# Kernel optimization log

Hardware: AMD Instinct MI355X
Metric: run time of the kernel (lower is better)

## Reference

```python
import jax, jax.numpy as jnp
import numpy as np
import math

B, S, H = 8, 1024, 1024
LN_EPS = 1e-5  # assumed epsilon of create_normalization_layer('layer_norm')


def setup_inputs() -> dict:
    key = jax.random.key(0)
    ks = jax.random.split(key, 6)
    context = jax.random.normal(ks[0], (B, S, H), dtype=jnp.float32)
    mask = jnp.ones((B, 1, S), dtype=jnp.int32)
    prior = jax.random.uniform(ks[1], (B, S, S), dtype=jnp.float32)
    # LayerNorm params
    gamma = jnp.ones((H,), dtype=jnp.float32)
    beta = jnp.zeros((H,), dtype=jnp.float32)
    # Dense projections (Glorot-like init)
    scale = 1.0 / np.sqrt(H)
    Wk = jax.random.normal(ks[2], (H, H), dtype=jnp.float32) * scale
    bk = jnp.zeros((H,), dtype=jnp.float32)
    Wq = jax.random.normal(ks[3], (H, H), dtype=jnp.float32) * scale
    bq = jnp.zeros((H,), dtype=jnp.float32)
    return {"context": context, "mask": mask, "prior": prior,
            "gamma": gamma, "beta": beta, "Wk": Wk, "bk": bk, "Wq": Wq, "bq": bq}


def reference(context, mask, prior, gamma, beta, Wk, bk, Wq, bq):
    dtype = context.dtype
    s = context.shape[1]
    hs = context.shape[2]
    i = jnp.arange(s)
    adj_upper = i[:, None] == (i[None, :] - 1)          # [S,S] superdiagonal
    adj_lower = i[:, None] == (i[None, :] + 1)          # subdiagonal
    adj_mask = adj_upper | adj_lower
    pad = mask[:, 0, :].astype(bool)                    # [B,S]
    pad2d = pad[:, :, None] & pad[:, None, :]           # [B,S,S]
    final_adj = adj_mask[None, :, :] & pad2d

    # LayerNorm over last axis
    mu = jnp.mean(context, axis=-1, keepdims=True)
    var = jnp.mean(jnp.square(context - mu), axis=-1, keepdims=True)
    cn = (context - mu) * jax.lax.rsqrt(var + LN_EPS) * gamma + beta

    k = cn @ Wk + bk                                    # [B,S,H]
    q = cn @ Wq + bq
    scores = jnp.einsum('bsh,bth->bst', q, k) / math.sqrt(hs)
    scores = jnp.where(final_adj, scores, jnp.asarray(-1e9, dtype))
    neibor = jax.nn.softmax(scores, axis=-1)
    neibor = jnp.sqrt(neibor * jnp.swapaxes(neibor, 1, 2) + 1e-9)
    neibor = prior + (1.0 - prior) * neibor

    triu = i[None, :] >= i[:, None]                     # [S,S] upper incl diag
    tri = triu.astype(dtype)
    b_eye = jnp.eye(s, dtype=bool)

    t = jnp.log(neibor + 1e-9)
    t = jnp.where(adj_upper[None, :, :], t, jnp.asarray(0.0, dtype))
    t = jnp.einsum('bij,jk->bik', t, tri)               # cumulative over cols
    g = jnp.exp(jnp.einsum('ij,bjk->bik', tri, t))      # hierarchical prefix product
    keep = jnp.logical_not(jnp.logical_xor(triu, b_eye))
    g = jnp.where(keep[None, :, :], g, jnp.asarray(0.0, dtype))
    neibor_diag = jnp.where(b_eye[None, :, :], jnp.asarray(1e-9, dtype), neibor)
    g = g + jnp.swapaxes(g, 1, 2) + neibor_diag
    g = g / (jnp.sum(g, axis=-1, keepdims=True) + 1e-9)

    f2d = pad2d.astype(dtype)
    g = g * f2d
    neibor = neibor * f2d
    return g, neibor
```

## Files before the change

### kernel.cpp

```cpp
#include <hip/hip_runtime.h>
#include <hip/hip_bf16.h>

#define SB 8
#define SS 1024
#define SH 1024
#define LN_EPS 1e-5f

typedef unsigned short u16;
typedef __attribute__((ext_vector_type(8))) short bf16x8;
typedef __attribute__((ext_vector_type(4))) float f32x4;

__device__ __forceinline__ u16 f2bf(float f) {
  __hip_bfloat16 h = __float2bfloat16(f);
  return *reinterpret_cast<u16*>(&h);
}
__device__ __forceinline__ float bf2f(u16 x) {
  unsigned v = ((unsigned)x) << 16;
  return __builtin_bit_cast(float, v);
}

__device__ __forceinline__ void gld16(const void* g, void* l) {
  __builtin_amdgcn_global_load_lds(
      (const __attribute__((address_space(1))) void*)g,
      (__attribute__((address_space(3))) void*)l, 16, 0, 0);
}

__global__ __launch_bounds__(256) void ln_cast(const float* __restrict__ x,
                                               const float* __restrict__ gamma,
                                               const float* __restrict__ beta,
                                               u16* __restrict__ cnb) {
  const int r = blockIdx.x;
  const int t = threadIdx.x;
  const int wave = t >> 6, lane = t & 63;
  const float* xr = x + (size_t)r * SH;
  float4 v = *(const float4*)(xr + 4 * t);

  __shared__ float p1[4], p2[4];
  float s = v.x + v.y + v.z + v.w;
#pragma unroll
  for (int off = 32; off > 0; off >>= 1) s += __shfl_down(s, off, 64);
  if (lane == 0) p1[wave] = s;
  __syncthreads();
  const float mu = (p1[0] + p1[1] + p1[2] + p1[3]) * (1.0f / SH);

  float d0 = v.x - mu, d1 = v.y - mu, d2 = v.z - mu, d3 = v.w - mu;
  float ss = d0 * d0 + d1 * d1 + d2 * d2 + d3 * d3;
#pragma unroll
  for (int off = 32; off > 0; off >>= 1) ss += __shfl_down(ss, off, 64);
  if (lane == 0) p2[wave] = ss;
  __syncthreads();
  const float rstd = rsqrtf((p2[0] + p2[1] + p2[2] + p2[3]) * (1.0f / SH) + LN_EPS);

  float4 gm = *(const float4*)(gamma + 4 * t);
  float4 bt = *(const float4*)(beta + 4 * t);
  ushort4 o;
  o.x = f2bf(d0 * rstd * gm.x + bt.x);
  o.y = f2bf(d1 * rstd * gm.y + bt.y);
  o.z = f2bf(d2 * rstd * gm.z + bt.z);
  o.w = f2bf(d3 * rstd * gm.w + bt.w);
  *(ushort4*)(cnb + (size_t)r * SH + 4 * t) = o;
}

__global__ __launch_bounds__(256) void wcast(const float* __restrict__ Wq,
                                             const float* __restrict__ Wk,
                                             u16* __restrict__ Wq_bf,
                                             u16* __restrict__ Wk_bf) {
  const size_t e = ((size_t)blockIdx.x * 256 + threadIdx.x) * 4;
  const size_t M = (size_t)SH * SH;
  const float* src;
  u16* dst;
  if (e < M) { src = Wq + e; dst = Wq_bf + e; }
  else       { src = Wk + (e - M); dst = Wk_bf + (e - M); }
  float4 v = *(const float4*)src;
  ushort4 o;
  o.x = f2bf(v.x); o.y = f2bf(v.y); o.z = f2bf(v.z); o.w = f2bf(v.w);
  *(ushort4*)dst = o;
}

__global__ __launch_bounds__(256) void wkbq_kernel(const float* __restrict__ Wk,
                                                   const float* __restrict__ bq,
                                                   float* __restrict__ wkbq) {
  const int wave = threadIdx.x >> 6, lane = threadIdx.x & 63;
  const int h = blockIdx.x * 4 + wave;
  const float* row = Wk + (size_t)h * SH;
  float s = 0.f;
#pragma unroll
  for (int v = 0; v < 4; ++v) {
    const int j = v * 256 + lane * 4;
    float4 w = *(const float4*)(row + j);
    float4 b = *(const float4*)(bq + j);
    s += w.x * b.x + w.y * b.y + w.z * b.z + w.w * b.w;
  }
#pragma unroll
  for (int off = 32; off > 0; off >>= 1) s += __shfl_down(s, off, 64);
  if (lane == 0) wkbq[h] = s;
}

__global__ __launch_bounds__(256) void zero_f32(float* __restrict__ p) {
  *(float4*)(p + ((size_t)blockIdx.x * 256 + threadIdx.x) * 4) =
      make_float4(0.f, 0.f, 0.f, 0.f);
}

#define BM 128
#define BN 128
#define BK 32
#define GK 1024
#define GN 1024

__global__ __launch_bounds__(256) void gemm_pt(const u16* __restrict__ A,
                                               const u16* __restrict__ Bt,
                                               u16* __restrict__ C) {
  __shared__ u16 As[BM * BK];
  __shared__ u16 Bs[BN * BK];
  const int tid = threadIdx.x;
  const int m0 = blockIdx.y * BM;
  const int n0 = blockIdx.x * BN;
  const int wave = tid >> 6, lane = tid & 63;
  const int wm = (wave & 1) * 64, wn = (wave >> 1) * 64;
  const int l15 = lane & 15, q = lane >> 4;

  f32x4 acc[4][4] = {};

  const int srow = tid >> 2;
  const int scol = 8 * (tid & 3);
  const u16* gA = A + (size_t)(m0 + srow) * GK + scol;
  const u16* gB = Bt + (size_t)(n0 + srow) * GK + scol;
  u16* lA = &As[srow * BK + scol];
  u16* lB = &Bs[srow * BK + scol];

  for (int k0 = 0; k0 < GK; k0 += BK) {
    __syncthreads();
    gld16(gA + k0, lA);
    gld16(gA + (size_t)64 * GK + k0, lA + 64 * BK);
    gld16(gB + k0, lB);
    gld16(gB + (size_t)64 * GK + k0, lB + 64 * BK);
    __syncthreads();

    bf16x8 af[4], bfr[4];
#pragma unroll
    for (int fm = 0; fm < 4; ++fm)
      af[fm] = *(const bf16x8*)&As[(wm + fm * 16 + l15) * BK + q * 8];
#pragma unroll
    for (int fn = 0; fn < 4; ++fn)
      bfr[fn] = *(const bf16x8*)&Bs[(wn + fn * 16 + l15) * BK + q * 8];
#pragma unroll
    for (int fm = 0; fm < 4; ++fm)
#pragma unroll
      for (int fn = 0; fn < 4; ++fn)
        acc[fm][fn] = __builtin_amdgcn_mfma_f32_16x16x32_bf16(
            af[fm], bfr[fn], acc[fm][fn], 0, 0, 0);
  }

#pragma unroll
  for (int fm = 0; fm < 4; ++fm)
#pragma unroll
    for (int fn = 0; fn < 4; ++fn) {
      const int row0 = m0 + wm + fm * 16 + q * 4;
      const int col = n0 + wn + fn * 16 + l15;
#pragma unroll
      for (int r = 0; r < 4; ++r)
        C[(size_t)(row0 + r) * GN + col] = f2bf(acc[fm][fn][r]);
    }
}

__global__ __launch_bounds__(256) void ugemm_fused(const u16* __restrict__ A,
                                                   const u16* __restrict__ Bt,
                                                   const u16* __restrict__ cnb,
                                                   float* __restrict__ du,
                                                   float* __restrict__ dd) {
  __shared__ u16 As[BM * BK];
  __shared__ u16 Bs[BN * BK];
  const int tid = threadIdx.x;
  const int m0 = blockIdx.y * BM;
  const int n0 = blockIdx.x * BN;
  const int wave = tid >> 6, lane = tid & 63;
  const int wm = (wave & 1) * 64, wn = (wave >> 1) * 64;
  const int l15 = lane & 15, q = lane >> 4;

  f32x4 acc[4][4] = {};

  const int srow = tid >> 2;
  const int scol = 8 * (tid & 3);
  const u16* gA = A + (size_t)(m0 + srow) * GK + scol;
  const u16* gB = Bt + (size_t)(n0 + srow) * GK + scol;
  u16* lA = &As[srow * BK + scol];
  u16* lB = &Bs[srow * BK + scol];

  for (int k0 = 0; k0 < GK; k0 += BK) {
    __syncthreads();
    gld16(gA + k0, lA);
    gld16(gA + (size_t)64 * GK + k0, lA + 64 * BK);
    gld16(gB + k0, lB);
    gld16(gB + (size_t)64 * GK + k0, lB + 64 * BK);
    __syncthreads();

    bf16x8 af[4], bfr[4];
#pragma unroll
    for (int fm = 0; fm < 4; ++fm)
      af[fm] = *(const bf16x8*)&As[(wm + fm * 16 + l15) * BK + q * 8];
#pragma unroll
    for (int fn = 0; fn < 4; ++fn)
      bfr[fn] = *(const bf16x8*)&Bs[(wn + fn * 16 + l15) * BK + q * 8];
#pragma unroll
    for (int fm = 0; fm < 4; ++fm)
#pragma unroll
      for (int fn = 0; fn < 4; ++fn)
        acc[fm][fn] = __builtin_amdgcn_mfma_f32_16x16x32_bf16(
            af[fm], bfr[fn], acc[fm][fn], 0, 0, 0);
  }

#pragma unroll
  for (int fm = 0; fm < 4; ++fm) {
#pragma unroll
    for (int rr = 0; rr < 4; ++rr) {
      const int r = m0 + wm + fm * 16 + q * 4 + rr;
      const int sl = r & (SS - 1);
      float sdu = 0.f, sdd = 0.f;
#pragma unroll
      for (int fn = 0; fn < 4; ++fn) {
        const int col = n0 + wn + fn * 16 + l15;
        const float a = acc[fm][fn][rr];
        if (sl < SS - 1) sdu += a * bf2f(cnb[(size_t)(r + 1) * SH + col]);
        if (sl > 0)      sdd += a * bf2f(cnb[(size_t)(r - 1) * SH + col]);
      }
#pragma unroll
      for (int m = 1; m < 16; m <<= 1) {
        sdu += __shfl_xor(sdu, m, 64);
        sdd += __shfl_xor(sdd, m, 64);
      }
      if (l15 == 0) {
        atomicAdd(&du[r], sdu);
        atomicAdd(&dd[r], sdd);
      }
    }
  }
}

__global__ __launch_bounds__(256) void wdot(const u16* __restrict__ cnb,
                                            const float* __restrict__ wkbq,
                                            float* __restrict__ wvec) {
  const int wave = threadIdx.x >> 6, lane = threadIdx.x & 63;
  const int r = blockIdx.x * 4 + wave;
  const u16* row = cnb + (size_t)r * SH;
  float s = 0.f;
#pragma unroll
  for (int v = 0; v < 4; ++v) {
    const int j = v * 256 + lane * 4;
    ushort4 c = *(const ushort4*)(row + j);
    float4 w = *(const float4*)(wkbq + j);
    s += bf2f(c.x) * w.x + bf2f(c.y) * w.y + bf2f(c.z) * w.z + bf2f(c.w) * w.w;
  }
#pragma unroll
  for (int off = 32; off > 0; off >>= 1) s += __shfl_down(s, off, 64);
  if (lane == 0) wvec[r] = s;
}

__global__ __launch_bounds__(256) void softmax2(const float* __restrict__ du,
                                                const float* __restrict__ dd,
                                                const float* __restrict__ wvec,
                                                float* __restrict__ pup,
                                                float* __restrict__ pdn) {
  const int r = blockIdx.x * 256 + threadIdx.x;
  const int s = r & (SS - 1);
  const bool has_up = (s < SS - 1), has_dn = (s > 0);
  const float scale = 0.03125f;
  float pu, pd;
  if (!has_dn) { pu = 1.f; pd = 0.f; }
  else if (!has_up) { pu = 0.f; pd = 1.f; }
  else {
    const float a = (du[r] + wvec[r + 1]) * scale;
    const float b = (dd[r] + wvec[r - 1]) * scale;
    const float m = fmaxf(a, b);
    const float eu = __expf(a - m), ed = __expf(b - m);
    const float inv = 1.f / (eu + ed);
    pu = eu * inv;
    pd = ed * inv;
  }
  pup[r] = pu;
  pdn[r] = pd;
}

__global__ __launch_bounds__(256) void rows_kernel(const float* __restrict__ prior,
                                                   const int* __restrict__ mask,
                                                   const float* __restrict__ pup,
                                                   const float* __restrict__ pdn,
                                                   float* __restrict__ g_out,
                                                   float* __restrict__ ne_out) {
  const int r = blockIdx.x;
  const int b = r >> 10, i = r & (SS - 1);
  const int t = threadIdx.x;
  const int wave = t >> 6, lane = t & 63;
  const float nbz = 3.1622776601683795e-5f;
  const float nb_im1 = (i >= 1) ? sqrtf(pup[r - 1] * pdn[r] + 1e-9f) : nbz;
  const float nb_ip1 = (i <= SS - 2) ? sqrtf(pup[r] * pdn[r + 1] + 1e-9f) : nbz;

  const float* prow = prior + (size_t)r * SS;
  float4 pr = *(const float4*)(prow + 4 * t);
  const int* mrow = mask + b * SS;
  const float padi = (mrow[i] != 0) ? 1.f : 0.f;
  int4 mk = *(const int4*)(mrow + 4 * t);

  float ne[4], gsum = 0.f;
#pragma unroll
  for (int v = 0; v < 4; ++v) {
    const int k = 4 * t + v;
    const float p = (&pr.x)[v];
    const float nb = (k == i - 1) ? nb_im1 : (k == i + 1) ? nb_ip1 : nbz;
    const float n = p + (1.f - p) * nb;
    ne[v] = n;
    gsum += (k == i) ? (2.f + 1e-9f) : (1.f + n);
  }

  __shared__ float part[4];
#pragma unroll
  for (int off = 32; off > 0; off >>= 1) gsum += __shfl_down(gsum, off, 64);
  if (lane == 0) part[wave] = gsum;
  __syncthreads();
  const float inv = 1.f / (part[0] + part[1] + part[2] + part[3] + 1e-9f);

  float4 go, no;
#pragma unroll
  for (int v = 0; v < 4; ++v) {
    const int k = 4 * t + v;
    const float padk = ((&mk.x)[v] != 0) ? 1.f : 0.f;
    const float f2 = padi * padk;
    const float gt = (k == i) ? (2.f + 1e-9f) : (1.f + ne[v]);
    (&go.x)[v] = gt * inv * f2;
    (&no.x)[v] = ne[v] * f2;
  }
  *(float4*)(g_out + (size_t)r * SS + 4 * t) = go;
  *(float4*)(ne_out + (size_t)r * SS + 4 * t) = no;
}

extern "C" void kernel_launch(void* const* d_in, const int* in_sizes, int n_in,
                              void* d_out, int out_size, void* d_ws, size_t ws_size,
                              hipStream_t stream) {
  const float* context = (const float*)d_in[0];
  const int* mask = (const int*)d_in[1];
  const float* prior = (const float*)d_in[2];
  const float* gamma = (const float*)d_in[3];
  const float* beta = (const float*)d_in[4];
  const float* Wk = (const float*)d_in[5];
  const float* bk = (const float*)d_in[6];
  const float* Wq = (const float*)d_in[7];
  const float* bq = (const float*)d_in[8];
  (void)bk;

  float* out_g = (float*)d_out;
  float* out_n = out_g + (size_t)SB * SS * SS;

  char* ws = (char*)d_ws;
  u16* cnb = (u16*)ws;
  u16* Wq_bf = (u16*)(ws + ((size_t)16 << 20));
  u16* Wk_bf = (u16*)(ws + ((size_t)18 << 20));
  u16* PT = (u16*)(ws + ((size_t)20 << 20));
  float* wkbq = (float*)(ws + ((size_t)22 << 20));
  float* wvec = (float*)(ws + ((size_t)23 << 20));
  float* du = (float*)(ws + ((size_t)24 << 20));
  float* dd = (float*)(ws + ((size_t)25 << 20));
  float* pup = (float*)(ws + ((size_t)26 << 20));
  float* pdn = (float*)(ws + ((size_t)27 << 20));

  ln_cast<<<SB * SS, 256, 0, stream>>>(context, gamma, beta, cnb);
  wcast<<<2048, 256, 0, stream>>>(Wq, Wk, Wq_bf, Wk_bf);
  wkbq_kernel<<<256, 256, 0, stream>>>(Wk, bq, wkbq);
  zero_f32<<<8, 256, 0, stream>>>(du);
  zero_f32<<<8, 256, 0, stream>>>(dd);
  gemm_pt<<<dim3(8, 8), 256, 0, stream>>>(Wk_bf, Wq_bf, PT);
  ugemm_fused<<<dim3(8, 64), 256, 0, stream>>>(cnb, PT, cnb, du, dd);
  wdot<<<SB * SS / 4, 256, 0, stream>>>(cnb, wkbq, wvec);
  softmax2<<<SB * SS / 256, 256, 0, stream>>>(du, dd, wvec, pup, pdn);
  rows_kernel<<<SB * SS, 256, 0, stream>>>(prior, mask, pup, pdn, out_g, out_n);
}
```

Baseline: 209.9 us.

## Fuse prep kernels and fold bias and softmax into GEMM and row kernels

Merges layernorm-cast, weight-cast, the Wk·bq reduction and accumulator zeroing into one prep kernel. The wkbq bias term is added per column inside the fused GEMM epilogue, which removes the separate wdot pass. The two-way softmax is recomputed inline in the row kernel, so softmax2 and the pup/pdn buffers are dropped. Kernel launches fall from ten to four, at the cost of some redundant exp work per row and a small change in where the bias term is added.

After: 196.5 us. -6.4%, faster.

```diff
diff --git a/kernel.cpp b/kernel.cpp
--- a/kernel.cpp
+++ b/kernel.cpp
@@ -25,80 +25,74 @@
       (__attribute__((address_space(3))) void*)l, 16, 0, 0);
 }
 
-__global__ __launch_bounds__(256) void ln_cast(const float* __restrict__ x,
-                                               const float* __restrict__ gamma,
-                                               const float* __restrict__ beta,
-                                               u16* __restrict__ cnb) {
-  const int r = blockIdx.x;
+__global__ __launch_bounds__(256) void prep(const float* __restrict__ x,
+                                            const float* __restrict__ gamma,
+                                            const float* __restrict__ beta,
+                                            const float* __restrict__ Wq,
+                                            const float* __restrict__ Wk,
+                                            const float* __restrict__ bq,
+                                            u16* __restrict__ cnb,
+                                            u16* __restrict__ Wq_bf,
+                                            u16* __restrict__ Wk_bf,
+                                            float* __restrict__ wkbq,
+                                            float* __restrict__ du,
+                                            float* __restrict__ dd) {
+  __shared__ float p1[4], p2[4];
+  const int blk = blockIdx.x;
   const int t = threadIdx.x;
   const int wave = t >> 6, lane = t & 63;
-  const float* xr = x + (size_t)r * SH;
-  float4 v = *(const float4*)(xr + 4 * t);
-
-  __shared__ float p1[4], p2[4];
-  float s = v.x + v.y + v.z + v.w;
-#pragma unroll
-  for (int off = 32; off > 0; off >>= 1) s += __shfl_down(s, off, 64);
-  if (lane == 0) p1[wave] = s;
-  __syncthreads();
-  const float mu = (p1[0] + p1[1] + p1[2] + p1[3]) * (1.0f / SH);
-
-  float d0 = v.x - mu, d1 = v.y - mu, d2 = v.z - mu, d3 = v.w - mu;
-  float ss = d0 * d0 + d1 * d1 + d2 * d2 + d3 * d3;
-#pragma unroll
-  for (int off = 32; off > 0; off >>= 1) ss += __shfl_down(ss, off, 64);
-  if (lane == 0) p2[wave] = ss;
-  __syncthreads();
-  const float rstd = rsqrtf((p2[0] + p2[1] + p2[2] + p2[3]) * (1.0f / SH) + LN_EPS);
-
-  float4 gm = *(const float4*)(gamma + 4 * t);
-  float4 bt = *(const float4*)(beta + 4 * t);
-  ushort4 o;
-  o.x = f2bf(d0 * rstd * gm.x + bt.x);
-  o.y = f2bf(d1 * rstd * gm.y + bt.y);
-  o.z = f2bf(d2 * rstd * gm.z + bt.z);
-  o.w = f2bf(d3 * rstd * gm.w + bt.w);
-  *(ushort4*)(cnb + (size_t)r * SH + 4 * t) = o;
-}
-
-__global__ __launch_bounds__(256) void wcast(const float* __restrict__ Wq,
-                                             const float* __restrict__ Wk,
-                                             u16* __restrict__ Wq_bf,
-                                             u16* __restrict__ Wk_bf) {
-  const size_t e = ((size_t)blockIdx.x * 256 + threadIdx.x) * 4;
-  const size_t M = (size_t)SH * SH;
-  const float* src;
-  u16* dst;
-  if (e < M) { src = Wq + e; dst = Wq_bf + e; }
-  else       { src = Wk + (e - M); dst = Wk_bf + (e - M); }
-  float4 v = *(const float4*)src;
-  ushort4 o;
-  o.x = f2bf(v.x); o.y = f2bf(v.y); o.z = f2bf(v.z); o.w = f2bf(v.w);
-  *(ushort4*)dst = o;
-}
-
-__global__ __launch_bounds__(256) void wkbq_kernel(const float* __restrict__ Wk,
-                                                   const float* __restrict__ bq,
-                                                   float* __restrict__ wkbq) {
-  const int wave = threadIdx.x >> 6, lane = threadIdx.x & 63;
-  const int h = blockIdx.x * 4 + wave;
-  const float* row = Wk + (size_t)h * SH;
-  float s = 0.f;
-#pragma unroll
-  for (int v = 0; v < 4; ++v) {
-    const int j = v * 256 + lane * 4;
-    float4 w = *(const float4*)(row + j);
-    float4 b = *(const float4*)(bq + j);
-    s += w.x * b.x + w.y * b.y + w.z * b.z + w.w * b.w;
-  }
-#pragma unroll
-  for (int off = 32; off > 0; off >>= 1) s += __shfl_down(s, off, 64);
-  if (lane == 0) wkbq[h] = s;
-}
-
-__global__ __launch_bounds__(256) void zero_f32(float* __restrict__ p) {
-  *(float4*)(p + ((size_t)blockIdx.x * 256 + threadIdx.x) * 4) =
-      make_float4(0.f, 0.f, 0.f, 0.f);
+
+  if (blk < SB * SS) {
+    const float* xr = x + (size_t)blk * SH;
+    float4 v = *(const float4*)(xr + 4 * t);
+
+    float s = v.x + v.y + v.z + v.w;
+#pragma unroll
+    for (int off = 32; off > 0; off >>= 1) s += __shfl_down(s, off, 64);
+    if (lane == 0) p1[wave] = s;
+    __syncthreads();
+    const float mu = (p1[0] + p1[1] + p1[2] + p1[3]) * (1.0f / SH);
+
+    float d0 = v.x - mu, d1 = v.y - mu, d2 = v.z - mu, d3 = v.w - mu;
+    float ss = d0 * d0 + d1 * d1 + d2 * d2 + d3 * d3;
+#pragma unroll
+    for (int off = 32; off > 0; off >>= 1) ss += __shfl_down(ss, off, 64);
+    if (lane == 0) p2[wave] = ss;
+    __syncthreads();
+    const float rstd =
+        rsqrtf((p2[0] + p2[1] + p2[2] + p2[3]) * (1.0f / SH) + LN_EPS);
+
+    float4 gm = *(const float4*)(gamma + 4 * t);
+    float4 bt = *(const float4*)(beta + 4 * t);
+    ushort4 o;
+    o.x = f2bf(d0 * rstd * gm.x + bt.x);
+    o.y = f2bf(d1 * rstd * gm.y + bt.y);
+    o.z = f2bf(d2 * rstd * gm.z + bt.z);
+    o.w = f2bf(d3 * rstd * gm.w + bt.w);
+    *(ushort4*)(cnb + (size_t)blk * SH + 4 * t) = o;
+    if (t == 0) {
+      du[blk] = 0.f;
+      dd[blk] = 0.f;
+    }
+  } else {
+    const int w = blk - SB * SS;
+    const bool is_q = (w < SH);
+    const float* src = is_q ? (Wq + (size_t)w * SH) : (Wk + (size_t)(w - SH) * SH);
+    u16* dst = is_q ? (Wq_bf + (size_t)w * SH) : (Wk_bf + (size_t)(w - SH) * SH);
+    float4 v = *(const float4*)(src + 4 * t);
+    ushort4 o;
+    o.x = f2bf(v.x); o.y = f2bf(v.y); o.z = f2bf(v.z); o.w = f2bf(v.w);
+    *(ushort4*)(dst + 4 * t) = o;
+    if (!is_q) {
+      float4 b = *(const float4*)(bq + 4 * t);
+      float s = v.x * b.x + v.y * b.y + v.z * b.z + v.w * b.w;
+#pragma unroll
+      for (int off = 32; off > 0; off >>= 1) s += __shfl_down(s, off, 64);
+      if (lane == 0) p1[wave] = s;
+      __syncthreads();
+      if (t == 0) wkbq[w - SH] = p1[0] + p1[1] + p1[2] + p1[3];
+    }
+  }
 }
 
 #define BM 128
@@ -166,6 +160,7 @@
 __global__ __launch_bounds__(256) void ugemm_fused(const u16* __restrict__ A,
                                                    const u16* __restrict__ Bt,
                                                    const u16* __restrict__ cnb,
+                                                   const float* __restrict__ wkbq,
                                                    float* __restrict__ du,
                                                    float* __restrict__ dd) {
   __shared__ u16 As[BM * BK];
@@ -209,6 +204,10 @@
             af[fm], bfr[fn], acc[fm][fn], 0, 0, 0);
   }
 
+  float wb[4];
+#pragma unroll
+  for (int fn = 0; fn < 4; ++fn) wb[fn] = wkbq[n0 + wn + fn * 16 + l15];
+
 #pragma unroll
   for (int fm = 0; fm < 4; ++fm) {
 #pragma unroll
@@ -219,7 +218,7 @@
 #pragma unroll
       for (int fn = 0; fn < 4; ++fn) {
         const int col = n0 + wn + fn * 16 + l15;
-        const float a = acc[fm][fn][rr];
+        const float a = acc[fm][fn][rr] + wb[fn];
         if (sl < SS - 1) sdu += a * bf2f(cnb[(size_t)(r + 1) * SH + col]);
         if (sl > 0)      sdd += a * bf2f(cnb[(size_t)(r - 1) * SH + col]);
       }
@@ -236,63 +235,48 @@
   }
 }
 
-__global__ __launch_bounds__(256) void wdot(const u16* __restrict__ cnb,
-                                            const float* __restrict__ wkbq,
-                                            float* __restrict__ wvec) {
-  const int wave = threadIdx.x >> 6, lane = threadIdx.x & 63;
-  const int r = blockIdx.x * 4 + wave;
-  const u16* row = cnb + (size_t)r * SH;
-  float s = 0.f;
-#pragma unroll
-  for (int v = 0; v < 4; ++v) {
-    const int j = v * 256 + lane * 4;
-    ushort4 c = *(const ushort4*)(row + j);
-    float4 w = *(const float4*)(wkbq + j);
-    s += bf2f(c.x) * w.x + bf2f(c.y) * w.y + bf2f(c.z) * w.z + bf2f(c.w) * w.w;
-  }
-#pragma unroll
-  for (int off = 32; off > 0; off >>= 1) s += __shfl_down(s, off, 64);
-  if (lane == 0) wvec[r] = s;
-}
-
-__global__ __launch_bounds__(256) void softmax2(const float* __restrict__ du,
-                                                const float* __restrict__ dd,
-                                                const float* __restrict__ wvec,
-                                                float* __restrict__ pup,
-                                                float* __restrict__ pdn) {
-  const int r = blockIdx.x * 256 + threadIdx.x;
-  const int s = r & (SS - 1);
-  const bool has_up = (s < SS - 1), has_dn = (s > 0);
-  const float scale = 0.03125f;
-  float pu, pd;
-  if (!has_dn) { pu = 1.f; pd = 0.f; }
-  else if (!has_up) { pu = 0.f; pd = 1.f; }
+__device__ __forceinline__ void soft2(const float* __restrict__ du,
+                                      const float* __restrict__ dd, int x,
+                                      float& pu, float& pd) {
+  const int sl = x & (SS - 1);
+  if (sl == 0) { pu = 1.f; pd = 0.f; }
+  else if (sl == SS - 1) { pu = 0.f; pd = 1.f; }
   else {
-    const float a = (du[r] + wvec[r + 1]) * scale;
-    const float b = (dd[r] + wvec[r - 1]) * scale;
+    const float a = du[x] * 0.03125f;
+    const float b = dd[x] * 0.03125f;
     const float m = fmaxf(a, b);
     const float eu = __expf(a - m), ed = __expf(b - m);
     const float inv = 1.f / (eu + ed);
     pu = eu * inv;
     pd = ed * inv;
   }
-  pup[r] = pu;
-  pdn[r] = pd;
-}
-
-__global__ __launch_bounds__(256) void rows_kernel(const float* __restrict__ prior,
-                                                   const int* __restrict__ mask,
-                                                   const float* __restrict__ pup,
-                                                   const float* __restrict__ pdn,
-                                                   float* __restrict__ g_out,
-                                                   float* __restrict__ ne_out) {
+}
+
+__global__ __launch_bounds__(256) void rows_fused(const float* __restrict__ prior,
+                                                  const int* __restrict__ mask,
+                                                  const float* __restrict__ du,
+                                                  const float* __restrict__ dd,
+                                                  float* __restrict__ g_out,
+                                                  float* __restrict__ ne_out) {
   const int r = blockIdx.x;
   const int b = r >> 10, i = r & (SS - 1);
   const int t = threadIdx.x;
   const int wave = t >> 6, lane = t & 63;
   const float nbz = 3.1622776601683795e-5f;
-  const float nb_im1 = (i >= 1) ? sqrtf(pup[r - 1] * pdn[r] + 1e-9f) : nbz;
-  const float nb_ip1 = (i <= SS - 2) ? sqrtf(pup[r] * pdn[r + 1] + 1e-9f) : nbz;
+
+  float nb_im1 = nbz, nb_ip1 = nbz;
+  if (i >= 1) {
+    float pu_m, pd_m, pu_c, pd_c;
+    soft2(du, dd, r - 1, pu_m, pd_m);
+    soft2(du, dd, r, pu_c, pd_c);
+    nb_im1 = sqrtf(pu_m * pd_c + 1e-9f);
+  }
+  if (i <= SS - 2) {
+    float pu_c, pd_c, pu_p, pd_p;
+    soft2(du, dd, r, pu_c, pd_c);
+    soft2(du, dd, r + 1, pu_p, pd_p);
+    nb_ip1 = sqrtf(pu_c * pd_p + 1e-9f);
+  }
 
   const float* prow = prior + (size_t)r * SS;
   float4 pr = *(const float4*)(prow + 4 * t);
@@ -355,20 +339,13 @@
   u16* Wk_bf = (u16*)(ws + ((size_t)18 << 20));
   u16* PT = (u16*)(ws + ((size_t)20 << 20));
   float* wkbq = (float*)(ws + ((size_t)22 << 20));
-  float* wvec = (float*)(ws + ((size_t)23 << 20));
-  float* du = (float*)(ws + ((size_t)24 << 20));
-  float* dd = (float*)(ws + ((size_t)25 << 20));
-  float* pup = (float*)(ws + ((size_t)26 << 20));
-  float* pdn = (float*)(ws + ((size_t)27 << 20));
-
-  ln_cast<<<SB * SS, 256, 0, stream>>>(context, gamma, beta, cnb);
-  wcast<<<2048, 256, 0, stream>>>(Wq, Wk, Wq_bf, Wk_bf);
-  wkbq_kernel<<<256, 256, 0, stream>>>(Wk, bq, wkbq);
-  zero_f32<<<8, 256, 0, stream>>>(du);
-  zero_f32<<<8, 256, 0, stream>>>(dd);
+  float* du = (float*)(ws + ((size_t)23 << 20));
+  float* dd = (float*)(ws + ((size_t)24 << 20));
+
+  prep<<<SB * SS + 2 * SH / 1, 256, 0, stream>>>(context, gamma, beta, Wq, Wk,
+                                                 bq, cnb, Wq_bf, Wk_bf, wkbq,
+                                                 du, dd);
   gemm_pt<<<dim3(8, 8), 256, 0, stream>>>(Wk_bf, Wq_bf, PT);
-  ugemm_fused<<<dim3(8, 64), 256, 0, stream>>>(cnb, PT, cnb, du, dd);
-  wdot<<<SB * SS / 4, 256, 0, stream>>>(cnb, wkbq, wvec);
-  softmax2<<<SB * SS / 256, 256, 0, stream>>>(du, dd, wvec, pup, pdn);
-  rows_kernel<<<SB * SS, 256, 0, stream>>>(prior, mask, pup, pdn, out_g, out_n);
-}
+  ugemm_fused<<<dim3(8, 64), 256, 0, stream>>>(cnb, PT, cnb, wkbq, du, dd);
+  rows_fused<<<SB * SS, 256, 0, stream>>>(prior, mask, du, dd, out_g, out_n);
+}
```
